# Kernel optimization log

Measured on AMD Instinct MI355X. Metric: run time of the kernel, lower is better.

Reference implementation:

```python
import jax, jax.numpy as jnp
import numpy as np

MARGIN = 0.3


def setup_inputs() -> dict:
    key = jax.random.key(0)
    k1, k2 = jax.random.split(key)
    inputs = jax.random.normal(k1, (8192, 128), dtype=jnp.float32)
    targets = jax.random.randint(k2, (8192,), 0, 512, dtype=jnp.int64)
    return {"inputs": inputs, "targets": targets}


def reference(inputs, targets):
    # inputs: [n, d], targets: [n]
    sq = jnp.sum(inputs * inputs, axis=1)  # [n]
    # dist[i,j] = ||x_i||^2 + ||x_j||^2 - 2 x_i . x_j
    dist = sq[:, None] + sq[None, :] - 2.0 * (inputs @ inputs.T)
    dist = jnp.sqrt(jnp.clip(dist, 1e-12, None))  # [n, n]
    mask = targets[:, None] == targets[None, :]  # True where same label
    # batch-hard mining: hardest positive (max) and hardest negative (min) per row.
    # Diagonal is always True, so every row has at least one positive.
    dist_ap = jnp.max(jnp.where(mask, dist, -jnp.inf), axis=1)  # [n]
    dist_an = jnp.min(jnp.where(mask, jnp.inf, dist), axis=1)  # [n]
    # MarginRankingLoss with y=1: mean(max(0, margin - (dist_an - dist_ap)))
    loss = jnp.mean(jnp.maximum(0.0, MARGIN - (dist_an - dist_ap)))
    prec = jnp.mean((dist_an > dist_ap).astype(jnp.float32))
    return loss, prec
```

## Files before the change

### kernel.cpp

```cpp
#include <hip/hip_runtime.h>
#include <hip/hip_bf16.h>
#include <math.h>

#define N 8192
#define D 128
#define MARGIN 0.3f

#define TI 128
#define TJ 128
#define JCH 8
#define JT_PER (N / (TJ * JCH))

typedef float f32x4 __attribute__((ext_vector_type(4)));
typedef short bf16x8 __attribute__((ext_vector_type(8)));
typedef unsigned short u16x8 __attribute__((ext_vector_type(8)));

#define AS1 __attribute__((address_space(1)))
#define AS3 __attribute__((address_space(3)))

__device__ inline void gload_lds16(const void* g, void* l) {
    __builtin_amdgcn_global_load_lds((AS1 void*)(void*)(g), (AS3 void*)(l), 16, 0, 0);
}

__device__ inline unsigned short f2bf(float f) {
    unsigned u = __float_as_uint(f);
    unsigned r = (u + 0x7FFFu + ((u >> 16) & 1u)) >> 16;
    return (unsigned short)r;
}

__global__ __launch_bounds__(256) void convert_kernel(const float* __restrict__ X,
                                                      unsigned short* __restrict__ Xb,
                                                      float* __restrict__ sq,
                                                      unsigned* __restrict__ ap2,
                                                      unsigned* __restrict__ an2) {
    int tid = threadIdx.x;
    int row = blockIdx.x * 16 + (tid >> 4);
    int l = tid & 15;
    const float4* p = reinterpret_cast<const float4*>(X + (size_t)row * D + l * 8);
    float4 u = p[0];
    float4 v = p[1];
    float s = u.x*u.x + u.y*u.y + u.z*u.z + u.w*u.w
            + v.x*v.x + v.y*v.y + v.z*v.z + v.w*v.w;
    u16x8 o;
    o[0] = f2bf(u.x); o[1] = f2bf(u.y); o[2] = f2bf(u.z); o[3] = f2bf(u.w);
    o[4] = f2bf(v.x); o[5] = f2bf(v.y); o[6] = f2bf(v.z); o[7] = f2bf(v.w);
    *reinterpret_cast<u16x8*>(Xb + (size_t)row * D + l * 8) = o;
    #pragma unroll
    for (int off = 8; off >= 1; off >>= 1) s += __shfl_xor(s, off);
    if (l == 0) {
        sq[row] = s;
        ap2[row] = 0u;
        an2[row] = 0x7F7F7F7Fu;
    }
}

__global__ __launch_bounds__(256, 2) void triplet_main(
        const unsigned short* __restrict__ Xb,
        const int* __restrict__ lbl,
        const float* __restrict__ sq,
        unsigned* __restrict__ ap2,
        unsigned* __restrict__ an2) {
    __shared__ unsigned short BufA[TI * D];
    __shared__ unsigned short BufB[TJ * D];
    __shared__ float sqj_s[2][TJ];
    __shared__ int   lblj_s[2][TJ];

    const int tid = threadIdx.x;
    const int w = tid >> 6;
    const int lane = tid & 63;
    const int wr = w >> 1;
    const int wc = w & 1;
    const int quad = lane >> 4;
    const int lx = lane & 15;
    const int i0 = blockIdx.x * TI;
    const int jbase = blockIdx.y * JT_PER * TJ;

    int lbl_i[16];
    #pragma unroll
    for (int t = 0; t < 4; ++t)
        #pragma unroll
        for (int v = 0; v < 4; ++v)
            lbl_i[t * 4 + v] = lbl[i0 + wr * 64 + t * 16 + quad * 4 + v];

    float m_ap[16], m_an[16];
    #pragma unroll
    for (int q = 0; q < 16; ++q) { m_ap[q] = -INFINITY; m_an[q] = INFINITY; }

    #pragma unroll
    for (int t = 0; t < 8; ++t) {
        int rbase = w * 32 + t * 4;
        int r = rbase + quad;
        int gc = lx ^ (r & 7);
        gload_lds16(Xb + (size_t)(i0 + r) * D + gc * 8, &BufA[rbase * D]);
    }
    #pragma unroll
    for (int t = 0; t < 8; ++t) {
        int rbase = w * 32 + t * 4;
        int r = rbase + quad;
        int gc = lx ^ (r & 7);
        gload_lds16(Xb + (size_t)(jbase + r) * D + gc * 8, &BufB[rbase * D]);
    }
    if (tid < TJ) { sqj_s[0][tid] = sq[jbase + tid]; lblj_s[0][tid] = lbl[jbase + tid]; }
    __syncthreads();

    bf16x8 af[4][4];
    #pragma unroll
    for (int ks = 0; ks < 4; ++ks)
        #pragma unroll
        for (int t = 0; t < 4; ++t) {
            int rA = wr * 64 + t * 16 + lx;
            int sc = (ks * 4 + quad) ^ (lx & 7);
            af[ks][t] = *reinterpret_cast<const bf16x8*>(&BufA[rA * D + sc * 8]);
        }
    __syncthreads();

    #pragma unroll 1
    for (int jt = 0; jt < JT_PER; ++jt) {
        const int cb = jt & 1;
        const unsigned short* cur = cb ? BufA : BufB;
        unsigned short* nxt = cb ? BufB : BufA;

        if (jt + 1 < JT_PER) {
            const int jb1 = jbase + (jt + 1) * TJ;
            #pragma unroll
            for (int t = 0; t < 8; ++t) {
                int rbase = w * 32 + t * 4;
                int r = rbase + quad;
                int gc = lx ^ (r & 7);
                gload_lds16(Xb + (size_t)(jb1 + r) * D + gc * 8, &nxt[rbase * D]);
            }
            if (tid < TJ) {
                sqj_s[1 - cb][tid] = sq[jb1 + tid];
                lblj_s[1 - cb][tid] = lbl[jb1 + tid];
            }
        }

        f32x4 acc[4][4];
        #pragma unroll
        for (int a = 0; a < 4; ++a)
            #pragma unroll
            for (int b = 0; b < 4; ++b)
                acc[a][b] = (f32x4){0.f, 0.f, 0.f, 0.f};

        #pragma unroll
        for (int ks = 0; ks < 4; ++ks) {
            bf16x8 bf[4];
            #pragma unroll
            for (int t = 0; t < 4; ++t) {
                int rB = wc * 64 + t * 16 + lx;
                int sc = (ks * 4 + quad) ^ (lx & 7);
                bf[t] = *reinterpret_cast<const bf16x8*>(&cur[rB * D + sc * 8]);
            }
            #pragma unroll
            for (int tr = 0; tr < 4; ++tr)
                #pragma unroll
                for (int tc = 0; tc < 4; ++tc)
                    acc[tr][tc] = __builtin_amdgcn_mfma_f32_16x16x32_bf16(
                        af[ks][tr], bf[tc], acc[tr][tc], 0, 0, 0);
        }

        #pragma unroll
        for (int tc = 0; tc < 4; ++tc) {
            int cj = wc * 64 + tc * 16 + lx;
            int ljv = lblj_s[cb][cj];
            float sjv = sqj_s[cb][cj];
            #pragma unroll
            for (int tr = 0; tr < 4; ++tr) {
                #pragma unroll
                for (int v = 0; v < 4; ++v) {
                    float val = fmaf(-2.f, acc[tr][tc][v], sjv);
                    bool same = (ljv == lbl_i[tr * 4 + v]);
                    int q = tr * 4 + v;
                    m_ap[q] = same ? fmaxf(m_ap[q], val) : m_ap[q];
                    m_an[q] = same ? m_an[q] : fminf(m_an[q], val);
                }
            }
        }
        __syncthreads();
    }

    #pragma unroll
    for (int off = 8; off >= 1; off >>= 1) {
        #pragma unroll
        for (int q = 0; q < 16; ++q) {
            m_ap[q] = fmaxf(m_ap[q], __shfl_xor(m_ap[q], off));
            m_an[q] = fminf(m_an[q], __shfl_xor(m_an[q], off));
        }
    }
    if (lx == 0) {
        #pragma unroll
        for (int t = 0; t < 4; ++t) {
            #pragma unroll
            for (int v = 0; v < 4; ++v) {
                int row = i0 + wr * 64 + t * 16 + quad * 4 + v;
                float si = sq[row];
                float vap = fmaxf(si + m_ap[t * 4 + v], 1e-12f);
                float van = fmaxf(si + m_an[t * 4 + v], 1e-12f);
                atomicMax(&ap2[row], __float_as_uint(vap));
                atomicMin(&an2[row], __float_as_uint(van));
            }
        }
    }
}

__global__ __launch_bounds__(1024) void finalize_kernel(const unsigned* __restrict__ ap2,
                                                        const unsigned* __restrict__ an2,
                                                        float* __restrict__ out) {
    int tid = threadIdx.x;
    float ls = 0.f, ps = 0.f;
    for (int row = tid; row < N; row += 1024) {
        float ap = sqrtf(__uint_as_float(ap2[row]));
        float an = sqrtf(__uint_as_float(an2[row]));
        ls += fmaxf(0.f, MARGIN - (an - ap));
        ps += (an > ap) ? 1.f : 0.f;
    }
    #pragma unroll
    for (int off = 32; off >= 1; off >>= 1) {
        ls += __shfl_xor(ls, off);
        ps += __shfl_xor(ps, off);
    }
    __shared__ float red[2][16];
    int w = tid >> 6;
    if ((tid & 63) == 0) { red[0][w] = ls; red[1][w] = ps; }
    __syncthreads();
    if (tid == 0) {
        float L = 0.f, P = 0.f;
        #pragma unroll
        for (int i = 0; i < 16; ++i) { L += red[0][i]; P += red[1][i]; }
        out[0] = L / (float)N;
        out[1] = P / (float)N;
    }
}

extern "C" void kernel_launch(void* const* d_in, const int* in_sizes, int n_in,
                              void* d_out, int out_size, void* d_ws, size_t ws_size,
                              hipStream_t stream) {
    const float* X = (const float*)d_in[0];
    const int* lbl = (const int*)d_in[1];
    float* out = (float*)d_out;

    float* sq = (float*)d_ws;
    unsigned* ap2 = (unsigned*)d_ws + N;
    unsigned* an2 = (unsigned*)d_ws + 2 * N;
    unsigned short* Xb = (unsigned short*)((char*)d_ws + 3 * N * sizeof(unsigned));

    convert_kernel<<<N / 16, 256, 0, stream>>>(X, Xb, sq, ap2, an2);
    dim3 grid(N / TI, JCH);
    triplet_main<<<grid, 256, 0, stream>>>(Xb, lbl, sq, ap2, an2);
    finalize_kernel<<<1, 1024, 0, stream>>>(ap2, an2, out);
}
```

Before: 94.51 us.

## Exploit distance-matrix symmetry by computing only upper-triangle tiles

The main kernel now processes only upper-triangular 128x128 tile pairs (bj >= bi), each block handling up to four j-tiles for one i-tile. For off-diagonal tiles, the column-wise hardest positive and negative are also reduced with cross-quad shuffles and merged into the j rows with atomics. This roughly halves the MFMA and tile-loading work, at the cost of more atomics, extra epilogue min/max work, and an uneven per-block tile count. Row squared norms are also kept in registers.

```diff
diff --git a/kernel.cpp b/kernel.cpp
--- a/kernel.cpp
+++ b/kernel.cpp
@@ -8,8 +8,8 @@
 
 #define TI 128
 #define TJ 128
-#define JCH 8
-#define JT_PER (N / (TJ * JCH))
+#define NTILE (N / 128)
+#define GRID_MAIN 544
 
 typedef float f32x4 __attribute__((ext_vector_type(4)));
 typedef short bf16x8 __attribute__((ext_vector_type(8)));
@@ -65,6 +65,16 @@
     __shared__ float sqj_s[2][TJ];
     __shared__ int   lblj_s[2][TJ];
 
+    int b = blockIdx.x;
+    int bi = 0;
+    for (;;) {
+        int cnt = (NTILE - bi + 3) >> 2;
+        if (b < cnt) break;
+        b -= cnt; ++bi;
+    }
+    const int bj0 = bi + (b << 2);
+    const int nt = min(4, NTILE - bj0);
+
     const int tid = threadIdx.x;
     const int w = tid >> 6;
     const int lane = tid & 63;
@@ -72,15 +82,18 @@
     const int wc = w & 1;
     const int quad = lane >> 4;
     const int lx = lane & 15;
-    const int i0 = blockIdx.x * TI;
-    const int jbase = blockIdx.y * JT_PER * TJ;
+    const int i0 = bi * TI;
 
     int lbl_i[16];
+    float sqi_r[16];
     #pragma unroll
     for (int t = 0; t < 4; ++t)
         #pragma unroll
-        for (int v = 0; v < 4; ++v)
-            lbl_i[t * 4 + v] = lbl[i0 + wr * 64 + t * 16 + quad * 4 + v];
+        for (int v = 0; v < 4; ++v) {
+            int row = i0 + wr * 64 + t * 16 + quad * 4 + v;
+            lbl_i[t * 4 + v] = lbl[row];
+            sqi_r[t * 4 + v] = sq[row];
+        }
 
     float m_ap[16], m_an[16];
     #pragma unroll
@@ -93,14 +106,15 @@
         int gc = lx ^ (r & 7);
         gload_lds16(Xb + (size_t)(i0 + r) * D + gc * 8, &BufA[rbase * D]);
     }
+    const int jb0 = bj0 * TJ;
     #pragma unroll
     for (int t = 0; t < 8; ++t) {
         int rbase = w * 32 + t * 4;
         int r = rbase + quad;
         int gc = lx ^ (r & 7);
-        gload_lds16(Xb + (size_t)(jbase + r) * D + gc * 8, &BufB[rbase * D]);
-    }
-    if (tid < TJ) { sqj_s[0][tid] = sq[jbase + tid]; lblj_s[0][tid] = lbl[jbase + tid]; }
+        gload_lds16(Xb + (size_t)(jb0 + r) * D + gc * 8, &BufB[rbase * D]);
+    }
+    if (tid < TJ) { sqj_s[0][tid] = sq[jb0 + tid]; lblj_s[0][tid] = lbl[jb0 + tid]; }
     __syncthreads();
 
     bf16x8 af[4][4];
@@ -115,13 +129,15 @@
     __syncthreads();
 
     #pragma unroll 1
-    for (int jt = 0; jt < JT_PER; ++jt) {
+    for (int jt = 0; jt < nt; ++jt) {
+        const int bj = bj0 + jt;
+        const int jb = bj * TJ;
         const int cb = jt & 1;
         const unsigned short* cur = cb ? BufA : BufB;
         unsigned short* nxt = cb ? BufB : BufA;
 
-        if (jt + 1 < JT_PER) {
-            const int jb1 = jbase + (jt + 1) * TJ;
+        if (jt + 1 < nt) {
+            const int jb1 = jb + TJ;
             #pragma unroll
             for (int t = 0; t < 8; ++t) {
                 int rbase = w * 32 + t * 4;
@@ -139,8 +155,8 @@
         #pragma unroll
         for (int a = 0; a < 4; ++a)
             #pragma unroll
-            for (int b = 0; b < 4; ++b)
-                acc[a][b] = (f32x4){0.f, 0.f, 0.f, 0.f};
+            for (int c = 0; c < 4; ++c)
+                acc[a][c] = (f32x4){0.f, 0.f, 0.f, 0.f};
 
         #pragma unroll
         for (int ks = 0; ks < 4; ++ks) {
@@ -159,20 +175,40 @@
                         af[ks][tr], bf[tc], acc[tr][tc], 0, 0, 0);
         }
 
+        const bool offdiag = (bj != bi);
         #pragma unroll
         for (int tc = 0; tc < 4; ++tc) {
             int cj = wc * 64 + tc * 16 + lx;
             int ljv = lblj_s[cb][cj];
             float sjv = sqj_s[cb][cj];
+            float mApJ = -INFINITY, mAnJ = INFINITY;
             #pragma unroll
             for (int tr = 0; tr < 4; ++tr) {
                 #pragma unroll
                 for (int v = 0; v < 4; ++v) {
-                    float val = fmaf(-2.f, acc[tr][tc][v], sjv);
-                    bool same = (ljv == lbl_i[tr * 4 + v]);
                     int q = tr * 4 + v;
-                    m_ap[q] = same ? fmaxf(m_ap[q], val) : m_ap[q];
-                    m_an[q] = same ? m_an[q] : fminf(m_an[q], val);
+                    float dot2 = -2.f * acc[tr][tc][v];
+                    float vi = sjv + dot2;
+                    float vj = sqi_r[q] + dot2;
+                    bool same = (ljv == lbl_i[q]);
+                    m_ap[q] = same ? fmaxf(m_ap[q], vi) : m_ap[q];
+                    m_an[q] = same ? m_an[q] : fminf(m_an[q], vi);
+                    mApJ = same ? fmaxf(mApJ, vj) : mApJ;
+                    mAnJ = same ? mAnJ : fminf(mAnJ, vj);
+                }
+            }
+            if (offdiag) {
+                #pragma unroll
+                for (int off = 16; off <= 32; off <<= 1) {
+                    mApJ = fmaxf(mApJ, __shfl_xor(mApJ, off));
+                    mAnJ = fminf(mAnJ, __shfl_xor(mAnJ, off));
+                }
+                if (quad == 0) {
+                    int rowg = jb + cj;
+                    float vap = fmaxf(sjv + mApJ, 1e-12f);
+                    float van = fmaxf(sjv + mAnJ, 1e-12f);
+                    atomicMax(&ap2[rowg], __float_as_uint(vap));
+                    atomicMin(&an2[rowg], __float_as_uint(van));
                 }
             }
         }
@@ -192,10 +228,10 @@
         for (int t = 0; t < 4; ++t) {
             #pragma unroll
             for (int v = 0; v < 4; ++v) {
+                int q = t * 4 + v;
                 int row = i0 + wr * 64 + t * 16 + quad * 4 + v;
-                float si = sq[row];
-                float vap = fmaxf(si + m_ap[t * 4 + v], 1e-12f);
-                float van = fmaxf(si + m_an[t * 4 + v], 1e-12f);
+                float vap = fmaxf(sqi_r[q] + m_ap[q], 1e-12f);
+                float van = fmaxf(sqi_r[q] + m_an[q], 1e-12f);
                 atomicMax(&ap2[row], __float_as_uint(vap));
                 atomicMin(&an2[row], __float_as_uint(van));
             }
@@ -245,7 +281,6 @@
     unsigned short* Xb = (unsigned short*)((char*)d_ws + 3 * N * sizeof(unsigned));
 
     convert_kernel<<<N / 16, 256, 0, stream>>>(X, Xb, sq, ap2, an2);
-    dim3 grid(N / TI, JCH);
-    triplet_main<<<grid, 256, 0, stream>>>(Xb, lbl, sq, ap2, an2);
+    triplet_main<<<GRID_MAIN, 256, 0, stream>>>(Xb, lbl, sq, ap2, an2);
     finalize_kernel<<<1, 1024, 0, stream>>>(ap2, an2, out);
 }
```

Result: slower. 118.7 us (+25.6%).
